# Optimization experiments

Hardware: AMD Instinct MI355X
Metric: run time of the kernel (lower is better)

Reference implementation:

```python
import jax, jax.numpy as jnp
import numpy as np

N_NODES = 50000
NEG_SLOPE = 0.2


def gat_conv(x, W, att_src, att_dst, b, src, dst, n):
    # x: [N, F_in], W: [F_in, H*C], att_*: [H, C], b: [H*C]
    H, C = att_src.shape
    h = (x @ W).reshape(n, H, C)                       # [N, H, C]
    a_s = (h * att_src).sum(-1)                        # [N, H]
    a_d = (h * att_dst).sum(-1)                        # [N, H]
    e = jax.nn.leaky_relu(a_s[src] + a_d[dst], NEG_SLOPE)  # [E, H]
    # segment softmax over destination node (every node has a self-loop)
    m = jax.ops.segment_max(e, dst, num_segments=n)    # [N, H]
    ex = jnp.exp(e - m[dst])
    denom = jax.ops.segment_sum(ex, dst, num_segments=n)
    alpha = ex / denom[dst]                            # [E, H]
    out = jax.ops.segment_sum(alpha[:, :, None] * h[src], dst, num_segments=n)
    return out.reshape(n, H * C) + b


def setup_inputs() -> dict:
    key = jax.random.key(0)
    ks = jax.random.split(key, 10)
    n, e = N_NODES, 1600000
    x = jax.random.normal(ks[0], (n, 128), dtype=jnp.float32)
    edge_index = jax.random.randint(ks[1], (2, e), 0, n, dtype=jnp.int64)
    s = 0.1
    return {
        "x": x,
        "edge_index": edge_index,
        "W1": jax.random.normal(ks[2], (128, 128), dtype=jnp.float32) * s,
        "att_src1": jax.random.normal(ks[3], (4, 32), dtype=jnp.float32) * s,
        "att_dst1": jax.random.normal(ks[4], (4, 32), dtype=jnp.float32) * s,
        "b1": jnp.zeros((128,), dtype=jnp.float32),
        "W2": jax.random.normal(ks[5], (128, 128), dtype=jnp.float32) * s,
        "att_src2": jax.random.normal(ks[6], (4, 32), dtype=jnp.float32) * s,
        "att_dst2": jax.random.normal(ks[7], (4, 32), dtype=jnp.float32) * s,
        "b2": jnp.zeros((128,), dtype=jnp.float32),
    }


def reference(x, edge_index, W1, att_src1, att_dst1, b1, W2, att_src2, att_dst2, b2):
    n = x.shape[0]
    loops = jnp.arange(n, dtype=edge_index.dtype)
    src = jnp.concatenate([edge_index[0], loops])  # add self-loops (PyG default)
    dst = jnp.concatenate([edge_index[1], loops])
    h = gat_conv(x, W1, att_src1, att_dst1, b1, src, dst, n)
    h = jax.nn.relu(h)
    h = gat_conv(h, W2, att_src2, att_dst2, b2, src, dst, n)
    return (h, h)
```

## Files before the change

### kernel.cpp

```cpp
#include <hip/hip_runtime.h>
#include <hip/hip_bf16.h>
#include <hip/hip_fp16.h>


#define FDIM 128
#define NHEAD 4
#define NB 512

typedef __attribute__((ext_vector_type(16))) float f32x16;
typedef __attribute__((ext_vector_type(8)))  short s16x8;

__device__ inline unsigned short f2bf(float f) {
    union { float f; unsigned u; } v; v.f = f;
    unsigned r = v.u + 0x7fff + ((v.u >> 16) & 1);
    return (unsigned short)(r >> 16);
}
__device__ inline float2 bf2f(unsigned v) {
    union { unsigned u; float f; } a, b;
    a.u = v << 16;
    b.u = v & 0xffff0000u;
    return make_float2(a.f, b.f);
}
__device__ inline void splitbf(float f, short* hi, short* lo) {
    unsigned u = __float_as_uint(f);
    float rem = f - __uint_as_float(u & 0xffff0000u);
    *hi = (short)(u >> 16);
    *lo = (short)(__float_as_uint(rem) >> 16);
}

__global__ __launch_bounds__(256) void prep_hist(const float* __restrict__ W1,
                                                 short* __restrict__ B1hi,
                                                 short* __restrict__ B1lo,
                                                 const float* __restrict__ W2,
                                                 short* __restrict__ B2hi,
                                                 short* __restrict__ B2lo,
                                                 const int* __restrict__ dst, int E,
                                                 unsigned long long magic,
                                                 int* __restrict__ bcnt) {
    __shared__ int sh[NB];
    const int t = threadIdx.x;
    const int b = blockIdx.x;
    if (b < 128) {
        const float* W = (b < 64) ? W1 : W2;
        short* Bhi = (b < 64) ? B1hi : B2hi;
        short* Blo = (b < 64) ? B1lo : B2lo;
        int e = (b & 63) * 256 + t;
        int k = e >> 7, n = e & 127;
        short hi, lo;
        splitbf(W[e], &hi, &lo);
        int idx = n * 128 + (((k >> 3) ^ (n & 15)) << 3) + (k & 7);
        Bhi[idx] = hi;
        Blo[idx] = lo;
        return;
    }
    for (int i = t; i < NB; i += 256) sh[i] = 0;
    __syncthreads();
    const int stride = (gridDim.x - 128) * 256;
    for (int i = (b - 128) * 256 + t; i < E; i += stride) {
        int bk = (int)(((unsigned long long)(unsigned)dst[i] * magic) >> 40);
        atomicAdd(&sh[bk], 1);
    }
    __syncthreads();
    for (int i = t; i < NB; i += 256)
        if (sh[i]) atomicAdd(&bcnt[i], sh[i]);
}

__global__ __launch_bounds__(256) void gemm_mfma(const float* __restrict__ A,
                                                 const short* __restrict__ Bghi,
                                                 const short* __restrict__ Bglo,
                                                 unsigned short* __restrict__ H,
                                                 const float* __restrict__ att_s,
                                                 const float* __restrict__ att_d,
                                                 float* __restrict__ a_s,
                                                 float* __restrict__ a_d, int M) {
    __shared__ short Bsm[2][16384];
    __shared__ float attsm[256];
    const int t = threadIdx.x;
    const int bm = blockIdx.x * 64;

    if (t < 128) attsm[t] = att_s[t];
    else         attsm[t] = att_d[t - 128];

    {
        const uint4* ghi = (const uint4*)Bghi;
        const uint4* glo = (const uint4*)Bglo;
        uint4* shi = (uint4*)&Bsm[0][0];
        uint4* slo = (uint4*)&Bsm[1][0];
        #pragma unroll
        for (int i = 0; i < 8; i++) {
            shi[t + i * 256] = ghi[t + i * 256];
            slo[t + i * 256] = glo[t + i * 256];
        }
    }

    const int lane = t & 63;
    const int w = t >> 6;
    const int wr = w >> 1, wc = w & 1;
    const int m  = lane & 31, h2 = lane >> 5;
    const int grow = bm + wr * 32 + m;

    s16x8 ahi[8], alo[8];
    {
        const bool ok = grow < M;
        const float* ap = A + (size_t)grow * 128 + 8 * h2;
        #pragma unroll
        for (int c = 0; c < 8; c++) {
            float ff[8];
            if (ok) {
                float4 f0 = *(const float4*)(ap + c * 16);
                float4 f1 = *(const float4*)(ap + c * 16 + 4);
                ff[0]=f0.x; ff[1]=f0.y; ff[2]=f0.z; ff[3]=f0.w;
                ff[4]=f1.x; ff[5]=f1.y; ff[6]=f1.z; ff[7]=f1.w;
            } else {
                #pragma unroll
                for (int j = 0; j < 8; j++) ff[j] = 0.f;
            }
            #pragma unroll
            for (int j = 0; j < 8; j++) {
                short hi, lo;
                splitbf(ff[j], &hi, &lo);
                ahi[c][j] = hi;
                alo[c][j] = lo;
            }
        }
    }
    __syncthreads();

    f32x16 acc[2];
    #pragma unroll
    for (int i = 0; i < 16; i++) { acc[0][i] = 0.f; acc[1][i] = 0.f; }

    #pragma unroll
    for (int ni = 0; ni < 2; ni++) {
        const int n = ni * 64 + wc * 32 + m;
        const int nbase = n * 128;
        #pragma unroll
        for (int c = 0; c < 8; c++) {
            int chunk8 = 2 * c + h2;
            int koff = ((chunk8 ^ (n & 15)) << 3);
            s16x8 bhi = *(const s16x8*)&Bsm[0][nbase + koff];
            s16x8 blo = *(const s16x8*)&Bsm[1][nbase + koff];
            acc[ni] = __builtin_amdgcn_mfma_f32_32x32x16_bf16(ahi[c], bhi, acc[ni], 0, 0, 0);
            acc[ni] = __builtin_amdgcn_mfma_f32_32x32x16_bf16(alo[c], bhi, acc[ni], 0, 0, 0);
            acc[ni] = __builtin_amdgcn_mfma_f32_32x32x16_bf16(ahi[c], blo, acc[ni], 0, 0, 0);
        }
    }

    __syncthreads();
    unsigned short* htile = (unsigned short*)&Bsm[0][0];
    #pragma unroll
    for (int ni = 0; ni < 2; ni++) {
        const int colg = ni * 64 + wc * 32 + m;
        #pragma unroll
        for (int r = 0; r < 16; r++) {
            int row = wr * 32 + (r & 3) + 8 * (r >> 2) + 4 * h2;
            htile[row * 128 + colg] = (short)f2bf(acc[ni][r]);
        }
    }
    __syncthreads();

    {
        const int r = t >> 2, q = t & 3;
        const int growr = bm + r;
        if (growr < M) {
            uint4 v0 = *(uint4*)&htile[r * 128 + q * 32];
            uint4 v1 = *(uint4*)&htile[r * 128 + q * 32 + 8];
            uint4 v2 = *(uint4*)&htile[r * 128 + q * 32 + 16];
            uint4 v3 = *(uint4*)&htile[r * 128 + q * 32 + 24];
            uint4* hg = (uint4*)(H + (size_t)growr * 128);
            hg[q * 4 + 0] = v0; hg[q * 4 + 1] = v1;
            hg[q * 4 + 2] = v2; hg[q * 4 + 3] = v3;
            unsigned uu[16] = {v0.x, v0.y, v0.z, v0.w, v1.x, v1.y, v1.z, v1.w,
                               v2.x, v2.y, v2.z, v2.w, v3.x, v3.y, v3.z, v3.w};
            float ps = 0.f, pd = 0.f;
            #pragma unroll
            for (int i = 0; i < 16; i++) {
                float2 f = bf2f(uu[i]);
                ps += f.x * attsm[q * 32 + 2 * i]       + f.y * attsm[q * 32 + 2 * i + 1];
                pd += f.x * attsm[128 + q * 32 + 2 * i] + f.y * attsm[128 + q * 32 + 2 * i + 1];
            }
            a_s[(size_t)q * M + growr] = ps;
            a_d[(size_t)q * M + growr] = pd;
        }
    }
}

__global__ __launch_bounds__(256) void bucket_scan(const int* __restrict__ bcnt,
                                                   int* __restrict__ bbase,
                                                   int* __restrict__ bcursor,
                                                   int* __restrict__ row_ptr,
                                                   int N, int E) {
    __shared__ int wsum[4];
    const int t = threadIdx.x, lane = t & 63, wid = t >> 6;
    int v0 = bcnt[2 * t], v1 = bcnt[2 * t + 1];
    int s = v0 + v1, incl = s;
    #pragma unroll
    for (int o = 1; o < 64; o <<= 1) {
        int u = __shfl_up(incl, o, 64);
        if (lane >= o) incl += u;
    }
    if (lane == 63) wsum[wid] = incl;
    __syncthreads();
    if (t == 0) {
        int a = 0;
        #pragma unroll
        for (int i = 0; i < 4; i++) { int x = wsum[i]; wsum[i] = a; a += x; }
    }
    __syncthreads();
    int excl = wsum[wid] + incl - s;
    bbase[2 * t] = excl;          bcursor[2 * t] = excl;
    bbase[2 * t + 1] = excl + v0; bcursor[2 * t + 1] = excl + v0;
    if (t == 0) { bbase[NB] = E; row_ptr[N] = E; }
}

__global__ __launch_bounds__(256) void partition(const int* __restrict__ src,
                                                 const int* __restrict__ dst, int E,
                                                 unsigned long long magic,
                                                 int* __restrict__ bcursor,
                                                 int2* __restrict__ ebuf) {
    __shared__ int shc[NB];
    __shared__ int shb[NB];
    __shared__ int shcur[NB];
    const int t = threadIdx.x;
    for (int i = t; i < NB; i += 256) shc[i] = 0;
    __syncthreads();
    const int e0 = blockIdx.x * 4096;
    int myb[16], mys[16], myd[16];
    #pragma unroll
    for (int u = 0; u < 16; u++) {
        int i = e0 + u * 256 + t;
        if (i < E) {
            mys[u] = src[i];
            myd[u] = dst[i];
            int b = (int)(((unsigned long long)(unsigned)myd[u] * magic) >> 40);
            myb[u] = b;
            atomicAdd(&shc[b], 1);
        } else myb[u] = -1;
    }
    __syncthreads();
    for (int i = t; i < NB; i += 256) {
        int c = shc[i];
        shcur[i] = 0;
        if (c) shb[i] = atomicAdd(&bcursor[i], c);
    }
    __syncthreads();
    #pragma unroll
    for (int u = 0; u < 16; u++) {
        if (myb[u] >= 0) {
            int o = atomicAdd(&shcur[myb[u]], 1);
            ebuf[shb[myb[u]] + o] = make_int2(mys[u], myd[u]);
        }
    }
}

__global__ __launch_bounds__(256) void build_bucket(const int2* __restrict__ ebuf,
                                                    const int* __restrict__ bbase,
                                                    int npb, int N,
                                                    int* __restrict__ row_ptr,
                                                    int* __restrict__ col) {
    __shared__ int degl[256];
    __shared__ int curl[256];
    const int b = blockIdx.x;
    const int t = threadIdx.x, lane = t & 63, wid = t >> 6;
    const int base = bbase[b];
    const int cnt = bbase[b + 1] - base;
    const int node0 = b * npb;
    for (int i = t; i < npb; i += 256) degl[i] = 0;
    __syncthreads();
    for (int i = t; i < cnt; i += 256) {
        int d = ebuf[base + i].y;
        atomicAdd(&degl[d - node0], 1);
    }
    __syncthreads();
    if (wid == 0) {
        int run = 0;
        for (int c = 0; c * 64 < npb; c++) {
            int idx = c * 64 + lane;
            int v = (idx < npb) ? degl[idx] : 0;
            int incl = v;
            #pragma unroll
            for (int o = 1; o < 64; o <<= 1) {
                int u = __shfl_up(incl, o, 64);
                if (lane >= o) incl += u;
            }
            int excl = incl - v + run;
            if (idx < npb) {
                curl[idx] = excl;
                int node = node0 + idx;
                if (node < N) row_ptr[node] = base + excl;
            }
            run += __shfl(incl, 63, 64);
        }
    }
    __syncthreads();
    for (int i = t; i < cnt; i += 256) {
        int2 ed = ebuf[base + i];
        int p = atomicAdd(&curl[ed.y - node0], 1);
        col[base + p] = ed.x;
    }
}

__global__ __launch_bounds__(64) void aggregate(const unsigned* __restrict__ h,
                                                const float* __restrict__ a_s,
                                                const float* __restrict__ a_d,
                                                const int* __restrict__ row_ptr,
                                                const int* __restrict__ col,
                                                const float* __restrict__ bias,
                                                float* __restrict__ out,
                                                float* __restrict__ out2,
                                                int n, int do_relu) {
    const int node = blockIdx.x;
    const int li = threadIdx.x;
    const int hd = li >> 4;
    const float* __restrict__ as_h = a_s + (size_t)hd * n;
    const float adv = a_d[(size_t)hd * n + node];

    float e = as_h[node] + adv;
    e = fmaxf(e, 0.2f * e);
    float den = __expf(e);
    float2 hv = bf2f(h[(size_t)node * 64 + li]);
    float num0 = den * hv.x, num1 = den * hv.y;

    const int beg = row_ptr[node], end = row_ptr[node + 1];
    int j = beg;
    for (; j + 8 <= end; j += 8) {
        int s[8];
        #pragma unroll
        for (int u = 0; u < 8; u++) s[u] = col[j + u];
        unsigned v[8];
        #pragma unroll
        for (int u = 0; u < 8; u++) v[u] = h[(size_t)s[u] * 64 + li];
        float av[8];
        #pragma unroll
        for (int u = 0; u < 8; u++) av[u] = as_h[s[u]];
        #pragma unroll
        for (int u = 0; u < 8; u++) {
            float ee = av[u] + adv;
            ee = fmaxf(ee, 0.2f * ee);
            float wgt = __expf(ee);
            den += wgt;
            float2 f = bf2f(v[u]);
            num0 += wgt * f.x;
            num1 += wgt * f.y;
        }
    }
    for (; j < end; j++) {
        int s = col[j];
        float ee = as_h[s] + adv;
        ee = fmaxf(ee, 0.2f * ee);
        float wgt = __expf(ee);
        den += wgt;
        float2 f = bf2f(h[(size_t)s * 64 + li]);
        num0 += wgt * f.x;
        num1 += wgt * f.y;
    }
    float2 bv = ((const float2*)bias)[li];
    float rd = 1.0f / den;
    float o0 = num0 * rd + bv.x;
    float o1 = num1 * rd + bv.y;
    if (do_relu) { o0 = fmaxf(o0, 0.f); o1 = fmaxf(o1, 0.f); }
    ((float2*)out)[(size_t)node * 64 + li] = make_float2(o0, o1);
    if (out2) ((float2*)out2)[(size_t)node * 64 + li] = make_float2(o0, o1);
}

extern "C" void kernel_launch(void* const* d_in, const int* in_sizes, int n_in,
                              void* d_out, int out_size, void* d_ws, size_t ws_size,
                              hipStream_t stream) {
    const float* x        = (const float*)d_in[0];
    const int*   edge     = (const int*)d_in[1];
    const float* W1       = (const float*)d_in[2];
    const float* att_s1   = (const float*)d_in[3];
    const float* att_d1   = (const float*)d_in[4];
    const float* b1       = (const float*)d_in[5];
    const float* W2       = (const float*)d_in[6];
    const float* att_s2   = (const float*)d_in[7];
    const float* att_d2   = (const float*)d_in[8];
    const float* b2       = (const float*)d_in[9];
    float* out = (float*)d_out;

    const int N = in_sizes[0] / FDIM;
    const int E = in_sizes[1] / 2;
    const int* src = edge;
    const int* dst = edge + E;

    const int npb = (N + NB - 1) / NB;
    const unsigned long long magic = ((1ull << 40) / (unsigned long long)npb) + 1;

    char* w = (char*)d_ws;
    size_t off = 0;
    auto alloc = [&](size_t bytes) { void* p = w + off; off = (off + bytes + 255) & ~(size_t)255; return p; };
    int*   row_ptr = (int*)alloc((size_t)(N + 1) * 4);
    int*   col     = (int*)alloc((size_t)E * 4);
    int*   bcnt    = (int*)alloc((size_t)NB * 4);
    int*   bbase   = (int*)alloc((size_t)(NB + 1) * 4);
    int*   bcursor = (int*)alloc((size_t)NB * 4);
    unsigned short* h = (unsigned short*)alloc((size_t)N * FDIM * 2);
    float* hx      = (float*)alloc((size_t)N * FDIM * 4);
    float* as1     = (float*)alloc((size_t)NHEAD * N * 4);
    float* ad1     = (float*)alloc((size_t)NHEAD * N * 4);
    float* as2     = (float*)alloc((size_t)NHEAD * N * 4);
    float* ad2     = (float*)alloc((size_t)NHEAD * N * 4);
    short* Bg1hi   = (short*)alloc((size_t)128 * 128 * 2);
    short* Bg1lo   = (short*)alloc((size_t)128 * 128 * 2);
    short* Bg2hi   = (short*)alloc((size_t)128 * 128 * 2);
    short* Bg2lo   = (short*)alloc((size_t)128 * 128 * 2);
    int2*  ebuf    = (int2*)hx;
    (void)ws_size;

    hipMemsetAsync(bcnt, 0, (size_t)NB * 4, stream);
    prep_hist<<<128 + 1024, 256, 0, stream>>>(W1, Bg1hi, Bg1lo, W2, Bg2hi, Bg2lo,
                                              dst, E, magic, bcnt);
    bucket_scan<<<1, 256, 0, stream>>>(bcnt, bbase, bcursor, row_ptr, N, E);
    partition<<<(E + 4095) / 4096, 256, 0, stream>>>(src, dst, E, magic, bcursor, ebuf);
    build_bucket<<<NB, 256, 0, stream>>>(ebuf, bbase, npb, N, row_ptr, col);

    const int gblocks = (N + 63) / 64;

    gemm_mfma<<<gblocks, 256, 0, stream>>>(x, Bg1hi, Bg1lo, h,
                                           att_s1, att_d1, as1, ad1, N);
    aggregate<<<N, 64, 0, stream>>>((const unsigned*)h, as1, ad1, row_ptr, col, b1,
                                    hx, nullptr, N, 1);

    gemm_mfma<<<gblocks, 256, 0, stream>>>(hx, Bg2hi, Bg2lo, h,
                                           att_s2, att_d2, as2, ad2, N);
    aggregate<<<N, 64, 0, stream>>>((const unsigned*)h, as2, ad2, row_ptr, col, b2,
                                    out, out + (size_t)N * FDIM, N, 0);
}
```

Before: 317.1 us.

## Build CSR via global per-node degree atomics and direct scatter instead of bucket partition

Replaces the two-pass bucket partition (edge buffer plus per-bucket local counting sort) with a global per-node degree histogram in the existing histogram kernel, a per-bucket row scan, and a direct scatter that takes a global atomic slot per edge. This removes the intermediate edge buffer writes and reads. In exchange it adds roughly 1.65M global atomics on the degree counters and another 1.65M on the cursors, with random access patterns. The order of neighbors within a row becomes nondeterministic, which can change floating-point summation order in the aggregation.

New measurement: 454.8 us. +43.4%, slower.

```diff
diff --git a/kernel.cpp b/kernel.cpp
--- a/kernel.cpp
+++ b/kernel.cpp
@@ -36,7 +36,8 @@
                                                  short* __restrict__ B2lo,
                                                  const int* __restrict__ dst, int E,
                                                  unsigned long long magic,
-                                                 int* __restrict__ bcnt) {
+                                                 int* __restrict__ bcnt,
+                                                 int* __restrict__ deg) {
     __shared__ int sh[NB];
     const int t = threadIdx.x;
     const int b = blockIdx.x;
@@ -57,7 +58,9 @@
     __syncthreads();
     const int stride = (gridDim.x - 128) * 256;
     for (int i = (b - 128) * 256 + t; i < E; i += stride) {
-        int bk = (int)(((unsigned long long)(unsigned)dst[i] * magic) >> 40);
+        int d = dst[i];
+        atomicAdd(&deg[d], 1);
+        int bk = (int)(((unsigned long long)(unsigned)d * magic) >> 40);
         atomicAdd(&sh[bk], 1);
     }
     __syncthreads();
@@ -187,7 +190,6 @@
 
 __global__ __launch_bounds__(256) void bucket_scan(const int* __restrict__ bcnt,
                                                    int* __restrict__ bbase,
-                                                   int* __restrict__ bcursor,
                                                    int* __restrict__ row_ptr,
                                                    int N, int E) {
     __shared__ int wsum[4];
@@ -208,95 +210,54 @@
     }
     __syncthreads();
     int excl = wsum[wid] + incl - s;
-    bbase[2 * t] = excl;          bcursor[2 * t] = excl;
-    bbase[2 * t + 1] = excl + v0; bcursor[2 * t + 1] = excl + v0;
+    bbase[2 * t] = excl;
+    bbase[2 * t + 1] = excl + v0;
     if (t == 0) { bbase[NB] = E; row_ptr[N] = E; }
 }
 
-__global__ __launch_bounds__(256) void partition(const int* __restrict__ src,
-                                                 const int* __restrict__ dst, int E,
-                                                 unsigned long long magic,
-                                                 int* __restrict__ bcursor,
-                                                 int2* __restrict__ ebuf) {
-    __shared__ int shc[NB];
-    __shared__ int shb[NB];
-    __shared__ int shcur[NB];
-    const int t = threadIdx.x;
-    for (int i = t; i < NB; i += 256) shc[i] = 0;
-    __syncthreads();
-    const int e0 = blockIdx.x * 4096;
-    int myb[16], mys[16], myd[16];
+__global__ __launch_bounds__(64) void row_scan(const int* __restrict__ deg,
+                                               const int* __restrict__ bbase,
+                                               int npb, int N,
+                                               int* __restrict__ row_ptr,
+                                               int* __restrict__ cursor) {
+    const int b = blockIdx.x;
+    const int lane = threadIdx.x;
+    const int node0 = b * npb;
+    const int base = bbase[b];
+    int run = 0;
+    for (int c = 0; c * 64 < npb; c++) {
+        int idx = c * 64 + lane;
+        int node = node0 + idx;
+        bool ok = (idx < npb) && (node < N);
+        int v = ok ? deg[node] : 0;
+        int incl = v;
+        #pragma unroll
+        for (int o = 1; o < 64; o <<= 1) {
+            int u = __shfl_up(incl, o, 64);
+            if (lane >= o) incl += u;
+        }
+        int excl = incl - v + run;
+        if (ok) {
+            row_ptr[node] = base + excl;
+            cursor[node]  = base + excl;
+        }
+        run += __shfl(incl, 63, 64);
+    }
+}
+
+__global__ __launch_bounds__(256) void scatter(const int* __restrict__ src,
+                                               const int* __restrict__ dst, int E,
+                                               int* __restrict__ cursor,
+                                               int* __restrict__ col) {
+    const int e0 = blockIdx.x * 4096 + threadIdx.x;
     #pragma unroll
     for (int u = 0; u < 16; u++) {
-        int i = e0 + u * 256 + t;
+        int i = e0 + u * 256;
         if (i < E) {
-            mys[u] = src[i];
-            myd[u] = dst[i];
-            int b = (int)(((unsigned long long)(unsigned)myd[u] * magic) >> 40);
-            myb[u] = b;
-            atomicAdd(&shc[b], 1);
-        } else myb[u] = -1;
-    }
-    __syncthreads();
-    for (int i = t; i < NB; i += 256) {
-        int c = shc[i];
-        shcur[i] = 0;
-        if (c) shb[i] = atomicAdd(&bcursor[i], c);
-    }
-    __syncthreads();
-    #pragma unroll
-    for (int u = 0; u < 16; u++) {
-        if (myb[u] >= 0) {
-            int o = atomicAdd(&shcur[myb[u]], 1);
-            ebuf[shb[myb[u]] + o] = make_int2(mys[u], myd[u]);
-        }
-    }
-}
-
-__global__ __launch_bounds__(256) void build_bucket(const int2* __restrict__ ebuf,
-                                                    const int* __restrict__ bbase,
-                                                    int npb, int N,
-                                                    int* __restrict__ row_ptr,
-                                                    int* __restrict__ col) {
-    __shared__ int degl[256];
-    __shared__ int curl[256];
-    const int b = blockIdx.x;
-    const int t = threadIdx.x, lane = t & 63, wid = t >> 6;
-    const int base = bbase[b];
-    const int cnt = bbase[b + 1] - base;
-    const int node0 = b * npb;
-    for (int i = t; i < npb; i += 256) degl[i] = 0;
-    __syncthreads();
-    for (int i = t; i < cnt; i += 256) {
-        int d = ebuf[base + i].y;
-        atomicAdd(&degl[d - node0], 1);
-    }
-    __syncthreads();
-    if (wid == 0) {
-        int run = 0;
-        for (int c = 0; c * 64 < npb; c++) {
-            int idx = c * 64 + lane;
-            int v = (idx < npb) ? degl[idx] : 0;
-            int incl = v;
-            #pragma unroll
-            for (int o = 1; o < 64; o <<= 1) {
-                int u = __shfl_up(incl, o, 64);
-                if (lane >= o) incl += u;
-            }
-            int excl = incl - v + run;
-            if (idx < npb) {
-                curl[idx] = excl;
-                int node = node0 + idx;
-                if (node < N) row_ptr[node] = base + excl;
-            }
-            run += __shfl(incl, 63, 64);
-        }
-    }
-    __syncthreads();
-    for (int i = t; i < cnt; i += 256) {
-        int2 ed = ebuf[base + i];
-        int p = atomicAdd(&curl[ed.y - node0], 1);
-        col[base + p] = ed.x;
+            int d = dst[i];
+            int p = atomicAdd(&cursor[d], 1);
+            col[p] = src[i];
+        }
     }
 }
 
@@ -393,7 +354,8 @@
     int*   col     = (int*)alloc((size_t)E * 4);
     int*   bcnt    = (int*)alloc((size_t)NB * 4);
     int*   bbase   = (int*)alloc((size_t)(NB + 1) * 4);
-    int*   bcursor = (int*)alloc((size_t)NB * 4);
+    int*   deg     = (int*)alloc((size_t)N * 4);
+    int*   cursor  = (int*)alloc((size_t)N * 4);
     unsigned short* h = (unsigned short*)alloc((size_t)N * FDIM * 2);
     float* hx      = (float*)alloc((size_t)N * FDIM * 4);
     float* as1     = (float*)alloc((size_t)NHEAD * N * 4);
@@ -404,15 +366,15 @@
     short* Bg1lo   = (short*)alloc((size_t)128 * 128 * 2);
     short* Bg2hi   = (short*)alloc((size_t)128 * 128 * 2);
     short* Bg2lo   = (short*)alloc((size_t)128 * 128 * 2);
-    int2*  ebuf    = (int2*)hx;
     (void)ws_size;
 
     hipMemsetAsync(bcnt, 0, (size_t)NB * 4, stream);
+    hipMemsetAsync(deg, 0, (size_t)N * 4, stream);
     prep_hist<<<128 + 1024, 256, 0, stream>>>(W1, Bg1hi, Bg1lo, W2, Bg2hi, Bg2lo,
-                                              dst, E, magic, bcnt);
-    bucket_scan<<<1, 256, 0, stream>>>(bcnt, bbase, bcursor, row_ptr, N, E);
-    partition<<<(E + 4095) / 4096, 256, 0, stream>>>(src, dst, E, magic, bcursor, ebuf);
-    build_bucket<<<NB, 256, 0, stream>>>(ebuf, bbase, npb, N, row_ptr, col);
+                                              dst, E, magic, bcnt, deg);
+    bucket_scan<<<1, 256, 0, stream>>>(bcnt, bbase, row_ptr, N, E);
+    row_scan<<<NB, 64, 0, stream>>>(deg, bbase, npb, N, row_ptr, cursor);
+    scatter<<<(E + 4095) / 4096, 256, 0, stream>>>(src, dst, E, cursor, col);
 
     const int gblocks = (N + 63) / 64;
 
```
